# Optimization experiments

Hardware: AMD Instinct MI355X
Metric: run time of the kernel (lower is better)

Reference implementation:

```python
import jax, jax.numpy as jnp
import numpy as np
import math

N = 4_194_304
EPS = 1e-07
CENTER_WEIGHT = 2.0
SIZE_WEIGHT = 1.0


def _make_boxes(kxy, kwh):
    # valid xyxy boxes: top-left in [0,600), width/height in [1,41)
    xy = jax.random.uniform(kxy, (N, 2), dtype=jnp.float32) * 600.0
    wh = jax.random.uniform(kwh, (N, 2), dtype=jnp.float32) * 40.0 + 1.0
    return jnp.concatenate([xy, xy + wh], axis=1)


def setup_inputs() -> dict:
    key = jax.random.key(0)
    k1, k2, k3, k4 = jax.random.split(key, 4)
    return {
        "pred_boxes": _make_boxes(k1, k2),
        "target_boxes": _make_boxes(k3, k4),
    }


def reference(pred_boxes, target_boxes):
    # Only the diagonal of the NxN pairwise CIoU tensors is used by the
    # original module, so compute the matched-pair terms directly (same math).
    px1, py1, px2, py2 = (pred_boxes[:, i] for i in range(4))
    tx1, ty1, tx2, ty2 = (target_boxes[:, i] for i in range(4))

    inter_w = jnp.clip(jnp.minimum(px2, tx2) - jnp.maximum(px1, tx1), 0.0)
    inter_h = jnp.clip(jnp.minimum(py2, ty2) - jnp.maximum(py1, ty1), 0.0)
    inter = inter_w * inter_h
    p_area = (px2 - px1) * (py2 - py1)
    t_area = (tx2 - tx1) * (ty2 - ty1)
    iou = inter / (p_area + t_area - inter + EPS)

    pcx, pcy = (px1 + px2) * 0.5, (py1 + py2) * 0.5
    tcx, tcy = (tx1 + tx2) * 0.5, (ty1 + ty2) * 0.5
    center_dist_sq = (pcx - tcx) ** 2 + (pcy - tcy) ** 2

    c_w = jnp.maximum(px2, tx2) - jnp.minimum(px1, tx1)
    c_h = jnp.maximum(py2, ty2) - jnp.minimum(py1, ty1)
    c_diag_sq = c_w ** 2 + c_h ** 2 + EPS  # bbox_iou adds eps here

    iou_term = 1.0 - iou
    # forward() adds eps again on top of c_diag_sq's eps (faithful to source)
    center_term = center_dist_sq / (c_diag_sq + EPS)

    pw, ph = px2 - px1, py2 - py1
    tw, th = tx2 - tx1, ty2 - ty1
    size_term = ((pw - tw) / (tw + EPS)) ** 2 + ((ph - th) / (th + EPS)) ** 2

    loss = iou_term + CENTER_WEIGHT * center_term + SIZE_WEIGHT * size_term
    return jnp.mean(loss)
```

## Files before the change

kernel.cpp:

```cpp
#include <hip/hip_runtime.h>


#define EPSF 1e-7f

__device__ __forceinline__ float wave_block_reduce(float acc, float* lds_ws) {
    #pragma unroll
    for (int off = 32; off > 0; off >>= 1)
        acc += __shfl_down(acc, off, 64);
    const int lane = threadIdx.x & 63;
    const int wave = threadIdx.x >> 6;
    if (lane == 0) lds_ws[wave] = acc;
    __syncthreads();
    float s = 0.f;
    if (threadIdx.x == 0) {
        const int nwaves = blockDim.x >> 6;
        for (int w = 0; w < nwaves; ++w) s += lds_ws[w];
    }
    return s;
}

__global__ void ciou_partial_kernel(const float4* __restrict__ pred,
                                    const float4* __restrict__ targ,
                                    float* __restrict__ partial, int n) {
    const int tid = blockIdx.x * blockDim.x + threadIdx.x;
    const int stride = gridDim.x * blockDim.x;
    float acc = 0.f;
    for (int i = tid; i < n; i += stride) {
        const float4 p = pred[i];
        const float4 t = targ[i];
        const float px1 = p.x, py1 = p.y, px2 = p.z, py2 = p.w;
        const float tx1 = t.x, ty1 = t.y, tx2 = t.z, ty2 = t.w;

        float iw = fminf(px2, tx2) - fmaxf(px1, tx1);
        float ih = fminf(py2, ty2) - fmaxf(py1, ty1);
        iw = fmaxf(iw, 0.f);
        ih = fmaxf(ih, 0.f);
        const float inter  = iw * ih;
        const float pw = px2 - px1, ph = py2 - py1;
        const float tw = tx2 - tx1, th = ty2 - ty1;
        const float p_area = pw * ph;
        const float t_area = tw * th;
        const float iou = inter / (p_area + t_area - inter + EPSF);

        const float dcx = 0.5f * ((px1 + px2) - (tx1 + tx2));
        const float dcy = 0.5f * ((py1 + py2) - (ty1 + ty2));
        const float center_dist_sq = dcx * dcx + dcy * dcy;
        const float cw = fmaxf(px2, tx2) - fminf(px1, tx1);
        const float ch = fmaxf(py2, ty2) - fminf(py1, ty1);
        const float c_diag_sq = cw * cw + ch * ch + EPSF;
        const float center_term = center_dist_sq / (c_diag_sq + EPSF);

        const float sw = (pw - tw) / (tw + EPSF);
        const float sh = (ph - th) / (th + EPSF);
        const float size_term = sw * sw + sh * sh;

        acc += (1.f - iou) + 2.f * center_term + size_term;
    }

    __shared__ float lds_ws[8];
    const float blk = wave_block_reduce(acc, lds_ws);
    if (threadIdx.x == 0) partial[blockIdx.x] = blk;
}

__global__ void ciou_final_kernel(const float* __restrict__ partial, int nparts,
                                  float* __restrict__ out, float inv_n) {
    float acc = 0.f;
    for (int i = threadIdx.x; i < nparts; i += blockDim.x)
        acc += partial[i];
    __shared__ float lds_ws[8];
    const float s = wave_block_reduce(acc, lds_ws);
    if (threadIdx.x == 0) out[0] = s * inv_n;
}

extern "C" void kernel_launch(void* const* d_in, const int* in_sizes, int n_in,
                              void* d_out, int out_size, void* d_ws, size_t ws_size,
                              hipStream_t stream) {
    const float4* pred = (const float4*)d_in[0];
    const float4* targ = (const float4*)d_in[1];
    float* out = (float*)d_out;
    float* partial = (float*)d_ws;

    const int n = in_sizes[0] / 4;
    const int block = 256;
    const int grid = 2048;

    ciou_partial_kernel<<<grid, block, 0, stream>>>(pred, targ, partial, n);
    ciou_final_kernel<<<1, block, 0, stream>>>(partial, grid, out, 1.0f / (float)n);
}
```

Measured before the change: 30.37 us.

## Unroll loads per thread with one-shot grid and use fast reciprocal

Replaces the fixed 2048-block grid-stride loop with a grid sized so each block handles 1024 elements. Each thread issues four float4 loads from both inputs before computing, to raise memory-level parallelism. Divisions are replaced with the hardware approximate reciprocal, which slightly changes precision. The final reduction now sums more partials (one per block).

```diff
diff --git a/kernel.cpp b/kernel.cpp
--- a/kernel.cpp
+++ b/kernel.cpp
@@ -2,6 +2,12 @@
 
 
 #define EPSF 1e-7f
+#define UNROLL 4
+#define BLOCK 256
+
+__device__ __forceinline__ float fast_rcp(float x) {
+    return __builtin_amdgcn_rcpf(x);
+}
 
 __device__ __forceinline__ float wave_block_reduce(float acc, float* lds_ws) {
     #pragma unroll
@@ -19,55 +25,73 @@
     return s;
 }
 
-__global__ void ciou_partial_kernel(const float4* __restrict__ pred,
-                                    const float4* __restrict__ targ,
-                                    float* __restrict__ partial, int n) {
-    const int tid = blockIdx.x * blockDim.x + threadIdx.x;
-    const int stride = gridDim.x * blockDim.x;
-    float acc = 0.f;
-    for (int i = tid; i < n; i += stride) {
-        const float4 p = pred[i];
-        const float4 t = targ[i];
-        const float px1 = p.x, py1 = p.y, px2 = p.z, py2 = p.w;
-        const float tx1 = t.x, ty1 = t.y, tx2 = t.z, ty2 = t.w;
+__device__ __forceinline__ float ciou_elem(float4 p, float4 t) {
+    const float px1 = p.x, py1 = p.y, px2 = p.z, py2 = p.w;
+    const float tx1 = t.x, ty1 = t.y, tx2 = t.z, ty2 = t.w;
 
-        float iw = fminf(px2, tx2) - fmaxf(px1, tx1);
-        float ih = fminf(py2, ty2) - fmaxf(py1, ty1);
-        iw = fmaxf(iw, 0.f);
-        ih = fmaxf(ih, 0.f);
-        const float inter  = iw * ih;
-        const float pw = px2 - px1, ph = py2 - py1;
-        const float tw = tx2 - tx1, th = ty2 - ty1;
-        const float p_area = pw * ph;
-        const float t_area = tw * th;
-        const float iou = inter / (p_area + t_area - inter + EPSF);
+    float iw = fminf(px2, tx2) - fmaxf(px1, tx1);
+    float ih = fminf(py2, ty2) - fmaxf(py1, ty1);
+    iw = fmaxf(iw, 0.f);
+    ih = fmaxf(ih, 0.f);
+    const float inter  = iw * ih;
+    const float pw = px2 - px1, ph = py2 - py1;
+    const float tw = tx2 - tx1, th = ty2 - ty1;
+    const float p_area = pw * ph;
+    const float t_area = tw * th;
+    const float iou = inter * fast_rcp(p_area + t_area - inter + EPSF);
 
-        const float dcx = 0.5f * ((px1 + px2) - (tx1 + tx2));
-        const float dcy = 0.5f * ((py1 + py2) - (ty1 + ty2));
-        const float center_dist_sq = dcx * dcx + dcy * dcy;
-        const float cw = fmaxf(px2, tx2) - fminf(px1, tx1);
-        const float ch = fmaxf(py2, ty2) - fminf(py1, ty1);
-        const float c_diag_sq = cw * cw + ch * ch + EPSF;
-        const float center_term = center_dist_sq / (c_diag_sq + EPSF);
+    const float dcx = 0.5f * ((px1 + px2) - (tx1 + tx2));
+    const float dcy = 0.5f * ((py1 + py2) - (ty1 + ty2));
+    const float center_dist_sq = dcx * dcx + dcy * dcy;
+    const float cw = fmaxf(px2, tx2) - fminf(px1, tx1);
+    const float ch = fmaxf(py2, ty2) - fminf(py1, ty1);
+    const float c_diag_sq = cw * cw + ch * ch + EPSF;
+    const float center_term = center_dist_sq * fast_rcp(c_diag_sq + EPSF);
 
-        const float sw = (pw - tw) / (tw + EPSF);
-        const float sh = (ph - th) / (th + EPSF);
-        const float size_term = sw * sw + sh * sh;
+    const float sw = (pw - tw) * fast_rcp(tw + EPSF);
+    const float sh = (ph - th) * fast_rcp(th + EPSF);
+    const float size_term = sw * sw + sh * sh;
 
-        acc += (1.f - iou) + 2.f * center_term + size_term;
+    return (1.f - iou) + 2.f * center_term + size_term;
+}
+
+__global__ __launch_bounds__(BLOCK) void ciou_partial_kernel(
+        const float4* __restrict__ pred,
+        const float4* __restrict__ targ,
+        float* __restrict__ partial, int n) {
+    const int base = blockIdx.x * (BLOCK * UNROLL) + threadIdx.x;
+
+    float4 p[UNROLL], t[UNROLL];
+    bool valid[UNROLL];
+    #pragma unroll
+    for (int u = 0; u < UNROLL; ++u) {
+        const int idx = base + u * BLOCK;
+        valid[u] = idx < n;
+        const int safe = valid[u] ? idx : 0;
+        p[u] = pred[safe];
+        t[u] = targ[safe];
     }
 
-    __shared__ float lds_ws[8];
+    float acc0 = 0.f, acc1 = 0.f;
+    #pragma unroll
+    for (int u = 0; u < UNROLL; u += 2) {
+        if (valid[u])     acc0 += ciou_elem(p[u],     t[u]);
+        if (valid[u + 1]) acc1 += ciou_elem(p[u + 1], t[u + 1]);
+    }
+    float acc = acc0 + acc1;
+
+    __shared__ float lds_ws[BLOCK / 64];
     const float blk = wave_block_reduce(acc, lds_ws);
     if (threadIdx.x == 0) partial[blockIdx.x] = blk;
 }
 
-__global__ void ciou_final_kernel(const float* __restrict__ partial, int nparts,
-                                  float* __restrict__ out, float inv_n) {
+__global__ __launch_bounds__(BLOCK) void ciou_final_kernel(
+        const float* __restrict__ partial, int nparts,
+        float* __restrict__ out, float inv_n) {
     float acc = 0.f;
     for (int i = threadIdx.x; i < nparts; i += blockDim.x)
         acc += partial[i];
-    __shared__ float lds_ws[8];
+    __shared__ float lds_ws[BLOCK / 64];
     const float s = wave_block_reduce(acc, lds_ws);
     if (threadIdx.x == 0) out[0] = s * inv_n;
 }
@@ -81,9 +105,9 @@
     float* partial = (float*)d_ws;
 
     const int n = in_sizes[0] / 4;
-    const int block = 256;
-    const int grid = 2048;
+    const int per_block = BLOCK * UNROLL;
+    const int grid = (n + per_block - 1) / per_block;
 
-    ciou_partial_kernel<<<grid, block, 0, stream>>>(pred, targ, partial, n);
-    ciou_final_kernel<<<1, block, 0, stream>>>(partial, grid, out, 1.0f / (float)n);
+    ciou_partial_kernel<<<grid, BLOCK, 0, stream>>>(pred, targ, partial, n);
+    ciou_final_kernel<<<1, BLOCK, 0, stream>>>(partial, grid, out, 1.0f / (float)n);
 }
```

Result: slower. 31.43 us (+3.5%).
